# Performance work log

Hardware: AMD Instinct MI355X
Metric: run time of the kernel (lower is better)

Reference implementation:

```python
import jax, jax.numpy as jnp
import numpy as np

TOP_K_PERCENT = 0.25  # top_k_percent_pixels from init_kwargs
B, C, H, W = 8, 19, 512, 1024


def setup_inputs() -> dict:
    key = jax.random.key(0)
    k1, k2 = jax.random.split(key)
    logits = jax.random.normal(k1, (B, C, H, W), dtype=jnp.float32)
    labels = jax.random.randint(k2, (B, H, W), 0, C)  # int labels, in-range
    return {"logits": logits, "labels": labels}


def reference(logits, labels):
    # loss_fn: per-pixel cross-entropy with reduction='none' -> [B, H, W]
    logZ = jax.nn.logsumexp(logits, axis=1)  # [B, H, W], stable softmax normalizer
    gathered = jnp.take_along_axis(logits, labels[:, None, :, :], axis=1)[:, 0]  # [B, H, W]
    loss = logZ - gathered  # per-pixel CE
    # get_topk_percent: flatten non-batch dims, keep top k = pct * num_pixels per row
    flat = loss.reshape(loss.shape[0], -1)  # [B, H*W]
    num_pixels = flat.shape[1]
    k = int(TOP_K_PERCENT * num_pixels)
    top_vals, _ = jax.lax.top_k(flat, k)  # [B, k]
    return top_vals.mean()
```

## Files before the change

kernel.cpp:

```cpp
#include <hip/hip_runtime.h>
#include <cstdint>

#define BB   8
#define CC   19
#define HWP  524288
#define NPIX 4194304
#define KSEL 131072
#define GRID 4096

#define H1_OFF   0
#define H2_OFF   (8*2048)
#define H3_OFF   (H2_OFF + 8*4096)
#define SEL1_OFF (H3_OFF + 8*256)
#define CNT1_OFF (SEL1_OFF + 8)
#define SEL2_OFF (CNT1_OFF + 8)
#define CNT2_OFF (SEL2_OFF + 8)
#define PAD_OFF  (CNT2_OFF + 8)
#define SUMA_OFF (PAD_OFF + 4)
#define CTRL_WORDS (SUMA_OFF + 16)
#define LOSS_BYTES (NPIX * 4)


__device__ __forceinline__ uint32_t block_incl_scan_u32(uint32_t v, volatile uint32_t* wt) {
    int lane = threadIdx.x & 63, wid = threadIdx.x >> 6;
    uint32_t inc = v;
#pragma unroll
    for (int off = 1; off < 64; off <<= 1) {
        uint32_t t = __shfl_up(inc, off);
        if (lane >= off) inc += t;
    }
    __syncthreads();
    if (lane == 63) wt[wid] = inc;
    __syncthreads();
    for (int w = 0; w < wid; w++) inc += wt[w];
    return inc;
}

__device__ __forceinline__ double block_reduce_double(double v, volatile double* dwt) {
    int lane = threadIdx.x & 63, wid = threadIdx.x >> 6;
#pragma unroll
    for (int off = 32; off > 0; off >>= 1) v += __shfl_down(v, off);
    __syncthreads();
    if (lane == 0) dwt[wid] = v;
    __syncthreads();
    return dwt[0] + dwt[1] + dwt[2] + dwt[3];
}

__device__ __forceinline__ void block_sum_atomic(double sum, double* dst, volatile double* dwt) {
    double t = block_reduce_double(sum, dwt);
    if (threadIdx.x == 0 && t != 0.0) atomicAdd(dst, t);
}


__global__ __launch_bounds__(256) void loss_hist1(
    const float* __restrict__ logits, const int* __restrict__ labels,
    float* __restrict__ loss, uint32_t* __restrict__ hist1)
{
    __shared__ uint32_t lh[2048];
    for (int i = threadIdx.x; i < 2048; i += 256) lh[i] = 0u;
    __syncthreads();

    int b = blockIdx.x >> 9;
    int pix0 = blockIdx.x * 1024 + threadIdx.x * 4;
    int prow = pix0 & (HWP - 1);

    const float4* lg = (const float4*)(logits + (size_t)b * CC * HWP + prow);
    float4 a[CC];
#pragma unroll
    for (int c = 0; c < CC; c++) a[c] = lg[(size_t)c * (HWP / 4)];

    int4 lab = *(const int4*)(labels + pix0);

    float mx0 = a[0].x, mx1 = a[0].y, mx2 = a[0].z, mx3 = a[0].w;
#pragma unroll
    for (int c = 1; c < CC; c++) {
        mx0 = fmaxf(mx0, a[c].x); mx1 = fmaxf(mx1, a[c].y);
        mx2 = fmaxf(mx2, a[c].z); mx3 = fmaxf(mx3, a[c].w);
    }
    float g0 = 0.f, g1 = 0.f, g2 = 0.f, g3 = 0.f;
    float e0 = 0.f, e1 = 0.f, e2 = 0.f, e3 = 0.f;
#pragma unroll
    for (int c = 0; c < CC; c++) {
        e0 += __expf(a[c].x - mx0); e1 += __expf(a[c].y - mx1);
        e2 += __expf(a[c].z - mx2); e3 += __expf(a[c].w - mx3);
        g0 = (lab.x == c) ? a[c].x : g0;
        g1 = (lab.y == c) ? a[c].y : g1;
        g2 = (lab.z == c) ? a[c].z : g2;
        g3 = (lab.w == c) ? a[c].w : g3;
    }
    float l0 = fmaxf(mx0 + __logf(e0) - g0, 0.f);
    float l1 = fmaxf(mx1 + __logf(e1) - g1, 0.f);
    float l2 = fmaxf(mx2 + __logf(e2) - g2, 0.f);
    float l3 = fmaxf(mx3 + __logf(e3) - g3, 0.f);

    float4 o; o.x = l0; o.y = l1; o.z = l2; o.w = l3;
    *(float4*)(loss + pix0) = o;

    atomicAdd(&lh[__float_as_uint(l0) >> 20], 1u);
    atomicAdd(&lh[__float_as_uint(l1) >> 20], 1u);
    atomicAdd(&lh[__float_as_uint(l2) >> 20], 1u);
    atomicAdd(&lh[__float_as_uint(l3) >> 20], 1u);

    __syncthreads();
    for (int i = threadIdx.x; i < 2048; i += 256) {
        uint32_t v = lh[i];
        if (v) atomicAdd(&hist1[b * 2048 + i], v);
    }
}


template <int NBINS>
__global__ __launch_bounds__(256) void scan_k(
    const uint32_t* __restrict__ hist, const uint32_t* __restrict__ cntPrev,
    uint32_t* __restrict__ selOut, uint32_t* __restrict__ cntOut)
{
    __shared__ uint32_t wt[4];
    constexpr int CH = NBINS / 256;
    int r = blockIdx.x;
    const uint32_t* hrow = hist + r * NBINS;
    int base = NBINS - CH * ((int)threadIdx.x + 1);
    uint32_t hloc[CH];
    uint32_t csum = 0;
#pragma unroll
    for (int i = 0; i < CH; i++) { hloc[i] = hrow[base + i]; csum += hloc[i]; }
    uint32_t incl = block_incl_scan_u32(csum, wt);
    uint32_t pre = incl - csum;
    uint32_t prev = cntPrev ? cntPrev[r] : 0u;
    uint32_t target = (uint32_t)KSEL - prev;
    if (pre < target && pre + csum >= target) {
        uint32_t cum = pre;
#pragma unroll
        for (int i = CH - 1; i >= 0; i--) {
            uint32_t h = hloc[i];
            if (cum + h >= target) { selOut[r] = (uint32_t)(base + i); cntOut[r] = prev + cum; break; }
            cum += h;
        }
    }
}


__global__ __launch_bounds__(256) void refine2(
    const float* __restrict__ loss, uint32_t* __restrict__ hist2,
    const uint32_t* __restrict__ sel1, double* __restrict__ sumAbove)
{
    __shared__ uint32_t lh[4096];
    __shared__ double dwt[4];
    for (int i = threadIdx.x; i < 4096; i += 256) lh[i] = 0u;
    __syncthreads();

    int b = blockIdx.x >> 9;
    uint32_t s1 = sel1[b];
    int pix0 = blockIdx.x * 1024 + threadIdx.x * 4;
    float4 v = *(const float4*)(loss + pix0);

    double sum = 0.0;
    {
        float vv[4] = {v.x, v.y, v.z, v.w};
#pragma unroll
        for (int j = 0; j < 4; j++) {
            uint32_t u = __float_as_uint(vv[j]);
            uint32_t t = u >> 20;
            if (t > s1) sum += (double)vv[j];
            else if (t == s1) atomicAdd(&lh[(u >> 8) & 0xFFFu], 1u);
        }
    }
    __syncthreads();
    block_sum_atomic(sum, &sumAbove[b], dwt);
    for (int i = threadIdx.x; i < 4096; i += 256) {
        uint32_t c = lh[i];
        if (c) atomicAdd(&hist2[b * 4096 + i], c);
    }
}


__global__ __launch_bounds__(256) void refine3(
    const float* __restrict__ loss, uint32_t* __restrict__ hist3,
    const uint32_t* __restrict__ sel1, const uint32_t* __restrict__ sel2,
    double* __restrict__ sumAbove)
{
    __shared__ uint32_t lh[256];
    __shared__ double dwt[4];
    lh[threadIdx.x] = 0u;
    __syncthreads();

    int b = blockIdx.x >> 9;
    uint32_t s1 = sel1[b], s2 = sel2[b];
    int pix0 = blockIdx.x * 1024 + threadIdx.x * 4;
    float4 v = *(const float4*)(loss + pix0);

    double sum = 0.0;
    {
        float vv[4] = {v.x, v.y, v.z, v.w};
#pragma unroll
        for (int j = 0; j < 4; j++) {
            uint32_t u = __float_as_uint(vv[j]);
            if ((u >> 20) == s1) {
                uint32_t mid = (u >> 8) & 0xFFFu;
                if (mid > s2) sum += (double)vv[j];
                else if (mid == s2) atomicAdd(&lh[u & 0xFFu], 1u);
            }
        }
    }
    __syncthreads();
    block_sum_atomic(sum, &sumAbove[b], dwt);
    {
        uint32_t c = lh[threadIdx.x];
        if (c) atomicAdd(&hist3[b * 256 + threadIdx.x], c);
    }
}


__global__ __launch_bounds__(256) void finalize_k(
    const uint32_t* __restrict__ hist3,
    const uint32_t* __restrict__ sel1, const uint32_t* __restrict__ sel2,
    const uint32_t* __restrict__ cnt2, const double* __restrict__ sumAbove,
    float* __restrict__ out)
{
    __shared__ uint32_t wt[4];
    __shared__ double dwt[4];
    double tot = 0.0;
    for (int r = 0; r < BB; r++) {
        int b3 = 255 - (int)threadIdx.x;
        uint32_t h = hist3[r * 256 + b3];
        uint32_t incl = block_incl_scan_u32(h, wt);
        uint32_t pre = incl - h;
        uint32_t rem = (uint32_t)KSEL - cnt2[r];
        uint32_t take = (rem > pre) ? ((rem - pre < h) ? (rem - pre) : h) : 0u;
        uint32_t P = (sel1[r] << 20) | (sel2[r] << 8) | (uint32_t)b3;
        double contrib = (double)take * (double)__uint_as_float(P);
        double s = block_reduce_double(contrib, dwt);
        if (threadIdx.x == 0) tot += s + sumAbove[r];
    }
    if (threadIdx.x == 0) out[0] = (float)(tot / ((double)BB * (double)KSEL));
}

extern "C" void kernel_launch(void* const* d_in, const int* in_sizes, int n_in,
                              void* d_out, int out_size, void* d_ws, size_t ws_size,
                              hipStream_t stream)
{
    const float* logits = (const float*)d_in[0];
    const int* labels   = (const int*)d_in[1];
    float* out          = (float*)d_out;

    char* ws = (char*)d_ws;
    float* loss      = (float*)ws;
    uint32_t* ctrl   = (uint32_t*)(ws + LOSS_BYTES);
    uint32_t* hist1  = ctrl + H1_OFF;
    uint32_t* hist2  = ctrl + H2_OFF;
    uint32_t* hist3  = ctrl + H3_OFF;
    uint32_t* sel1   = ctrl + SEL1_OFF;
    uint32_t* cnt1   = ctrl + CNT1_OFF;
    uint32_t* sel2   = ctrl + SEL2_OFF;
    uint32_t* cnt2   = ctrl + CNT2_OFF;
    double* sumAbove = (double*)(ctrl + SUMA_OFF);

    (void)hipMemsetAsync(ctrl, 0, CTRL_WORDS * sizeof(uint32_t), stream);
    loss_hist1<<<GRID, 256, 0, stream>>>(logits, labels, loss, hist1);
    scan_k<2048><<<BB, 256, 0, stream>>>(hist1, nullptr, sel1, cnt1);
    refine2<<<GRID, 256, 0, stream>>>(loss, hist2, sel1, sumAbove);
    scan_k<4096><<<BB, 256, 0, stream>>>(hist2, cnt1, sel2, cnt2);
    refine3<<<GRID, 256, 0, stream>>>(loss, hist3, sel1, sel2, sumAbove);
    finalize_k<<<1, 256, 0, stream>>>(hist3, sel1, sel2, cnt2, sumAbove, out);
}
```

Measured before the change: 536.0 us.

## Fuse loss and radix-select passes into one cooperative persistent kernel

Replaces the six-launch pipeline with a single cooperative kernel of 512 blocks. Each block keeps its 8192 per-pixel losses in registers, and the stages are separated by grid.sync, so the loss buffer is never written to or re-read from global memory. Every block redoes the histogram scan for its own row instead of launching separate scan kernels, and the control words are zeroed inside the kernel rather than by a memset. The trade-offs are heavy register pressure from holding 19 float4 logits plus 8 float4 losses per thread, fewer blocks in flight to hide memory latency, and the cost of several grid-wide barriers; the old multi-kernel path stays as a fallback if the cooperative launch fails.

```diff
diff --git a/kernel.cpp b/kernel.cpp
--- a/kernel.cpp
+++ b/kernel.cpp
@@ -1,13 +1,23 @@
 #include <hip/hip_runtime.h>
+#include <hip/hip_cooperative_groups.h>
 #include <cstdint>
+
+namespace cg = cooperative_groups;
 
 #define BB   8
 #define CC   19
 #define HWP  524288
 #define NPIX 4194304
 #define KSEL 131072
+
+#define CNBLK 512
+#define CBPR  64
+#define CNTHR 256
+#define CGRP  8
+
 #define GRID 4096
 
+#define LOSS_BYTES (NPIX * 4)
 #define H1_OFF   0
 #define H2_OFF   (8*2048)
 #define H3_OFF   (H2_OFF + 8*4096)
@@ -16,9 +26,8 @@
 #define SEL2_OFF (CNT1_OFF + 8)
 #define CNT2_OFF (SEL2_OFF + 8)
 #define PAD_OFF  (CNT2_OFF + 8)
-#define SUMA_OFF (PAD_OFF + 4)
+#define SUMA_OFF (PAD_OFF + 2)
 #define CTRL_WORDS (SUMA_OFF + 16)
-#define LOSS_BYTES (NPIX * 4)
 
 
 __device__ __forceinline__ uint32_t block_incl_scan_u32(uint32_t v, volatile uint32_t* wt) {
@@ -49,6 +58,186 @@
 __device__ __forceinline__ void block_sum_atomic(double sum, double* dst, volatile double* dwt) {
     double t = block_reduce_double(sum, dwt);
     if (threadIdx.x == 0 && t != 0.0) atomicAdd(dst, t);
+}
+
+template <int NBINS>
+__device__ __forceinline__ void row_select(
+    const uint32_t* __restrict__ hrow, uint32_t prev,
+    volatile uint32_t* wt, volatile uint32_t* shSel, volatile uint32_t* shCnt,
+    uint32_t& sel, uint32_t& cnt)
+{
+    constexpr int CH = NBINS / 256;
+    int base = NBINS - CH * ((int)threadIdx.x + 1);
+    uint32_t hloc[CH];
+    uint32_t csum = 0;
+#pragma unroll
+    for (int i = 0; i < CH; i++) { hloc[i] = hrow[base + i]; csum += hloc[i]; }
+    uint32_t incl = block_incl_scan_u32(csum, wt);
+    uint32_t pre = incl - csum;
+    uint32_t target = (uint32_t)KSEL - prev;
+    if (pre < target && pre + csum >= target) {
+        uint32_t cum = pre;
+#pragma unroll
+        for (int i = CH - 1; i >= 0; i--) {
+            uint32_t h = hloc[i];
+            if (cum + h >= target) { *shSel = (uint32_t)(base + i); *shCnt = prev + cum; break; }
+            cum += h;
+        }
+    }
+    __syncthreads();
+    sel = *shSel; cnt = *shCnt;
+}
+
+
+__global__ __launch_bounds__(CNTHR, 2) void topk_ce_coop(
+    const float* __restrict__ logits, const int* __restrict__ labels,
+    uint32_t* __restrict__ ctrl, float* __restrict__ out)
+{
+    cg::grid_group grid = cg::this_grid();
+    __shared__ uint32_t lh[4096];
+    __shared__ uint32_t wt[4];
+    __shared__ double dwt[4];
+    __shared__ uint32_t shSel, shCnt;
+
+    uint32_t* hist1 = ctrl + H1_OFF;
+    uint32_t* hist2 = ctrl + H2_OFF;
+    uint32_t* hist3 = ctrl + H3_OFF;
+    uint32_t* sel1g = ctrl + SEL1_OFF;
+    uint32_t* sel2g = ctrl + SEL2_OFF;
+    uint32_t* cnt2g = ctrl + CNT2_OFF;
+    double* sumAbove = (double*)(ctrl + SUMA_OFF);
+
+    const int tid = threadIdx.x;
+    const int b = (int)blockIdx.x >> 6;
+    const int rowblk = (int)blockIdx.x & (CBPR - 1);
+
+    for (int i = (int)blockIdx.x * CNTHR + tid; i < CTRL_WORDS; i += CNBLK * CNTHR)
+        ctrl[i] = 0u;
+    for (int i = tid; i < 2048; i += CNTHR) lh[i] = 0u;
+    __syncthreads();
+
+    const size_t rowbase = (size_t)b * CC * HWP;
+    const size_t labbase = (size_t)b * HWP;
+    const int prow0 = rowblk * (CNTHR * 4 * CGRP) + tid * 4;
+
+    float4 lr[CGRP];
+#pragma unroll
+    for (int g = 0; g < CGRP; g++) {
+        const int prow = prow0 + g * (CNTHR * 4);
+        const float4* lg = (const float4*)(logits + rowbase + prow);
+        const int4 lab = *(const int4*)(labels + labbase + prow);
+        float4 a[CC];
+#pragma unroll
+        for (int c = 0; c < CC; c++) a[c] = lg[(size_t)c * (HWP / 4)];
+
+        float mx0 = a[0].x, mx1 = a[0].y, mx2 = a[0].z, mx3 = a[0].w;
+#pragma unroll
+        for (int c = 1; c < CC; c++) {
+            mx0 = fmaxf(mx0, a[c].x); mx1 = fmaxf(mx1, a[c].y);
+            mx2 = fmaxf(mx2, a[c].z); mx3 = fmaxf(mx3, a[c].w);
+        }
+        float g0 = 0.f, g1 = 0.f, g2 = 0.f, g3 = 0.f;
+        float e0 = 0.f, e1 = 0.f, e2 = 0.f, e3 = 0.f;
+#pragma unroll
+        for (int c = 0; c < CC; c++) {
+            e0 += __expf(a[c].x - mx0); e1 += __expf(a[c].y - mx1);
+            e2 += __expf(a[c].z - mx2); e3 += __expf(a[c].w - mx3);
+            g0 = (lab.x == c) ? a[c].x : g0;
+            g1 = (lab.y == c) ? a[c].y : g1;
+            g2 = (lab.z == c) ? a[c].z : g2;
+            g3 = (lab.w == c) ? a[c].w : g3;
+        }
+        float l0 = fmaxf(mx0 + __logf(e0) - g0, 0.f);
+        float l1 = fmaxf(mx1 + __logf(e1) - g1, 0.f);
+        float l2 = fmaxf(mx2 + __logf(e2) - g2, 0.f);
+        float l3 = fmaxf(mx3 + __logf(e3) - g3, 0.f);
+        lr[g] = make_float4(l0, l1, l2, l3);
+
+        atomicAdd(&lh[__float_as_uint(l0) >> 20], 1u);
+        atomicAdd(&lh[__float_as_uint(l1) >> 20], 1u);
+        atomicAdd(&lh[__float_as_uint(l2) >> 20], 1u);
+        atomicAdd(&lh[__float_as_uint(l3) >> 20], 1u);
+    }
+    __syncthreads();
+    grid.sync();
+    for (int i = tid; i < 2048; i += CNTHR) {
+        uint32_t v = lh[i];
+        if (v) atomicAdd(&hist1[b * 2048 + i], v);
+    }
+    grid.sync();
+
+    uint32_t sel1v, cnt1v;
+    row_select<2048>(hist1 + b * 2048, 0u, wt, &shSel, &shCnt, sel1v, cnt1v);
+    __syncthreads();
+    for (int i = tid; i < 4096; i += CNTHR) lh[i] = 0u;
+    __syncthreads();
+
+    double sum = 0.0;
+#pragma unroll
+    for (int g = 0; g < CGRP; g++) {
+        float vv[4] = {lr[g].x, lr[g].y, lr[g].z, lr[g].w};
+#pragma unroll
+        for (int j = 0; j < 4; j++) {
+            uint32_t u = __float_as_uint(vv[j]);
+            uint32_t t = u >> 20;
+            if (t > sel1v) sum += (double)vv[j];
+            else if (t == sel1v) atomicAdd(&lh[(u >> 8) & 0xFFFu], 1u);
+        }
+    }
+    __syncthreads();
+    block_sum_atomic(sum, &sumAbove[b], dwt);
+    for (int i = tid; i < 4096; i += CNTHR) {
+        uint32_t v = lh[i];
+        if (v) atomicAdd(&hist2[b * 4096 + i], v);
+    }
+    if (rowblk == 0 && tid == 0) sel1g[b] = sel1v;
+    grid.sync();
+
+    uint32_t sel2v, cnt2v;
+    row_select<4096>(hist2 + b * 4096, cnt1v, wt, &shSel, &shCnt, sel2v, cnt2v);
+    __syncthreads();
+    lh[tid] = 0u;
+    __syncthreads();
+
+    double sum2 = 0.0;
+#pragma unroll
+    for (int g = 0; g < CGRP; g++) {
+        float vv[4] = {lr[g].x, lr[g].y, lr[g].z, lr[g].w};
+#pragma unroll
+        for (int j = 0; j < 4; j++) {
+            uint32_t u = __float_as_uint(vv[j]);
+            if ((u >> 20) == sel1v) {
+                uint32_t mid = (u >> 8) & 0xFFFu;
+                if (mid > sel2v) sum2 += (double)vv[j];
+                else if (mid == sel2v) atomicAdd(&lh[u & 0xFFu], 1u);
+            }
+        }
+    }
+    __syncthreads();
+    block_sum_atomic(sum2, &sumAbove[b], dwt);
+    {
+        uint32_t c = lh[tid];
+        if (c) atomicAdd(&hist3[b * 256 + tid], c);
+    }
+    if (rowblk == 0 && tid == 0) { sel2g[b] = sel2v; cnt2g[b] = cnt2v; }
+    grid.sync();
+
+    if (blockIdx.x == 0) {
+        double tot = 0.0;
+        for (int r = 0; r < BB; r++) {
+            int b3 = 255 - tid;
+            uint32_t h = hist3[r * 256 + b3];
+            uint32_t incl = block_incl_scan_u32(h, wt);
+            uint32_t pre = incl - h;
+            uint32_t rem = (uint32_t)KSEL - cnt2g[r];
+            uint32_t take = (rem > pre) ? ((rem - pre < h) ? (rem - pre) : h) : 0u;
+            uint32_t P = (sel1g[r] << 20) | (sel2g[r] << 8) | (uint32_t)b3;
+            double contrib = (double)take * (double)__uint_as_float(P);
+            double s = block_reduce_double(contrib, dwt);
+            if (tid == 0) tot += s + sumAbove[r];
+        }
+        if (tid == 0) out[0] = (float)(tot / ((double)BB * (double)KSEL));
+    }
 }
 
 
@@ -108,7 +297,6 @@
     }
 }
 
-
 template <int NBINS>
 __global__ __launch_bounds__(256) void scan_k(
     const uint32_t* __restrict__ hist, const uint32_t* __restrict__ cntPrev,
@@ -138,7 +326,6 @@
     }
 }
 
-
 __global__ __launch_bounds__(256) void refine2(
     const float* __restrict__ loss, uint32_t* __restrict__ hist2,
     const uint32_t* __restrict__ sel1, double* __restrict__ sumAbove)
@@ -171,7 +358,6 @@
         if (c) atomicAdd(&hist2[b * 4096 + i], c);
     }
 }
-
 
 __global__ __launch_bounds__(256) void refine3(
     const float* __restrict__ loss, uint32_t* __restrict__ hist3,
@@ -208,7 +394,6 @@
         if (c) atomicAdd(&hist3[b * 256 + threadIdx.x], c);
     }
 }
-
 
 __global__ __launch_bounds__(256) void finalize_k(
     const uint32_t* __restrict__ hist3,
@@ -254,6 +439,18 @@
     uint32_t* cnt2   = ctrl + CNT2_OFF;
     double* sumAbove = (double*)(ctrl + SUMA_OFF);
 
+    {
+        const float* a0 = logits;
+        const int*   a1 = labels;
+        uint32_t*    a2 = ctrl;
+        float*       a3 = out;
+        void* args[4] = { (void*)&a0, (void*)&a1, (void*)&a2, (void*)&a3 };
+        if (hipLaunchCooperativeKernel(topk_ce_coop, dim3(CNBLK), dim3(CNTHR),
+                                       args, 0, stream) == hipSuccess)
+            return;
+        (void)hipGetLastError();
+    }
+
     (void)hipMemsetAsync(ctrl, 0, CTRL_WORDS * sizeof(uint32_t), stream);
     loss_hist1<<<GRID, 256, 0, stream>>>(logits, labels, loss, hist1);
     scan_k<2048><<<BB, 256, 0, stream>>>(hist1, nullptr, sel1, cnt1);
```

After: 669.4 us. 1.25x slower.

## Fold histogram scan-select into each refine kernel, dropping separate scan launches

Applied to the files above, without the earlier changes.

Removes the two small 8-block scan_k launches. Each block of the refine kernels now redundantly scans its row's histogram to find the selected bin, and block 0 of each row writes sel/cnt for later stages. This cuts two kernel launches and their serialization gaps, at the cost of every one of 4096 blocks re-reading and scanning a 2048- or 4096-entry histogram row. The SUMA offset shift keeps the double array 8-byte aligned.

```diff
diff --git a/kernel.cpp b/kernel.cpp
--- a/kernel.cpp
+++ b/kernel.cpp
@@ -16,7 +16,7 @@
 #define SEL2_OFF (CNT1_OFF + 8)
 #define CNT2_OFF (SEL2_OFF + 8)
 #define PAD_OFF  (CNT2_OFF + 8)
-#define SUMA_OFF (PAD_OFF + 4)
+#define SUMA_OFF (PAD_OFF + 2)
 #define CTRL_WORDS (SUMA_OFF + 16)
 #define LOSS_BYTES (NPIX * 4)
 
@@ -49,6 +49,34 @@
 __device__ __forceinline__ void block_sum_atomic(double sum, double* dst, volatile double* dwt) {
     double t = block_reduce_double(sum, dwt);
     if (threadIdx.x == 0 && t != 0.0) atomicAdd(dst, t);
+}
+
+template <int NBINS>
+__device__ __forceinline__ void row_select(
+    const uint32_t* __restrict__ hrow, uint32_t prev,
+    volatile uint32_t* wt, volatile uint32_t* shSel, volatile uint32_t* shCnt,
+    uint32_t& sel, uint32_t& cnt)
+{
+    constexpr int CH = NBINS / 256;
+    int base = NBINS - CH * ((int)threadIdx.x + 1);
+    uint32_t hloc[CH];
+    uint32_t csum = 0;
+#pragma unroll
+    for (int i = 0; i < CH; i++) { hloc[i] = hrow[base + i]; csum += hloc[i]; }
+    uint32_t incl = block_incl_scan_u32(csum, wt);
+    uint32_t pre = incl - csum;
+    uint32_t target = (uint32_t)KSEL - prev;
+    if (pre < target && pre + csum >= target) {
+        uint32_t cum = pre;
+#pragma unroll
+        for (int i = CH - 1; i >= 0; i--) {
+            uint32_t h = hloc[i];
+            if (cum + h >= target) { *shSel = (uint32_t)(base + i); *shCnt = prev + cum; break; }
+            cum += h;
+        }
+    }
+    __syncthreads();
+    sel = *shSel; cnt = *shCnt;
 }
 
 
@@ -109,47 +137,27 @@
 }
 
 
-template <int NBINS>
-__global__ __launch_bounds__(256) void scan_k(
-    const uint32_t* __restrict__ hist, const uint32_t* __restrict__ cntPrev,
-    uint32_t* __restrict__ selOut, uint32_t* __restrict__ cntOut)
-{
+__global__ __launch_bounds__(256) void refine2s(
+    const float* __restrict__ loss, const uint32_t* __restrict__ hist1,
+    uint32_t* __restrict__ hist2,
+    uint32_t* __restrict__ sel1g, uint32_t* __restrict__ cnt1g,
+    double* __restrict__ sumAbove)
+{
+    __shared__ uint32_t lh[4096];
     __shared__ uint32_t wt[4];
-    constexpr int CH = NBINS / 256;
-    int r = blockIdx.x;
-    const uint32_t* hrow = hist + r * NBINS;
-    int base = NBINS - CH * ((int)threadIdx.x + 1);
-    uint32_t hloc[CH];
-    uint32_t csum = 0;
-#pragma unroll
-    for (int i = 0; i < CH; i++) { hloc[i] = hrow[base + i]; csum += hloc[i]; }
-    uint32_t incl = block_incl_scan_u32(csum, wt);
-    uint32_t pre = incl - csum;
-    uint32_t prev = cntPrev ? cntPrev[r] : 0u;
-    uint32_t target = (uint32_t)KSEL - prev;
-    if (pre < target && pre + csum >= target) {
-        uint32_t cum = pre;
-#pragma unroll
-        for (int i = CH - 1; i >= 0; i--) {
-            uint32_t h = hloc[i];
-            if (cum + h >= target) { selOut[r] = (uint32_t)(base + i); cntOut[r] = prev + cum; break; }
-            cum += h;
-        }
-    }
-}
-
-
-__global__ __launch_bounds__(256) void refine2(
-    const float* __restrict__ loss, uint32_t* __restrict__ hist2,
-    const uint32_t* __restrict__ sel1, double* __restrict__ sumAbove)
-{
-    __shared__ uint32_t lh[4096];
     __shared__ double dwt[4];
+    __shared__ uint32_t shSel, shCnt;
     for (int i = threadIdx.x; i < 4096; i += 256) lh[i] = 0u;
     __syncthreads();
 
     int b = blockIdx.x >> 9;
-    uint32_t s1 = sel1[b];
+    int rowblk = blockIdx.x & 511;
+
+    uint32_t s1, c1;
+    row_select<2048>(hist1 + b * 2048, 0u, wt, &shSel, &shCnt, s1, c1);
+    if (rowblk == 0 && threadIdx.x == 0) { sel1g[b] = s1; cnt1g[b] = c1; }
+    __syncthreads();
+
     int pix0 = blockIdx.x * 1024 + threadIdx.x * 4;
     float4 v = *(const float4*)(loss + pix0);
 
@@ -173,18 +181,30 @@
 }
 
 
-__global__ __launch_bounds__(256) void refine3(
-    const float* __restrict__ loss, uint32_t* __restrict__ hist3,
-    const uint32_t* __restrict__ sel1, const uint32_t* __restrict__ sel2,
+__global__ __launch_bounds__(256) void refine3s(
+    const float* __restrict__ loss, const uint32_t* __restrict__ hist2,
+    uint32_t* __restrict__ hist3,
+    const uint32_t* __restrict__ sel1g, const uint32_t* __restrict__ cnt1g,
+    uint32_t* __restrict__ sel2g, uint32_t* __restrict__ cnt2g,
     double* __restrict__ sumAbove)
 {
     __shared__ uint32_t lh[256];
+    __shared__ uint32_t wt[4];
     __shared__ double dwt[4];
+    __shared__ uint32_t shSel, shCnt;
     lh[threadIdx.x] = 0u;
     __syncthreads();
 
     int b = blockIdx.x >> 9;
-    uint32_t s1 = sel1[b], s2 = sel2[b];
+    int rowblk = blockIdx.x & 511;
+    uint32_t s1 = sel1g[b];
+    uint32_t c1 = cnt1g[b];
+
+    uint32_t s2, c2;
+    row_select<4096>(hist2 + b * 4096, c1, wt, &shSel, &shCnt, s2, c2);
+    if (rowblk == 0 && threadIdx.x == 0) { sel2g[b] = s2; cnt2g[b] = c2; }
+    __syncthreads();
+
     int pix0 = blockIdx.x * 1024 + threadIdx.x * 4;
     float4 v = *(const float4*)(loss + pix0);
 
@@ -256,9 +276,7 @@
 
     (void)hipMemsetAsync(ctrl, 0, CTRL_WORDS * sizeof(uint32_t), stream);
     loss_hist1<<<GRID, 256, 0, stream>>>(logits, labels, loss, hist1);
-    scan_k<2048><<<BB, 256, 0, stream>>>(hist1, nullptr, sel1, cnt1);
-    refine2<<<GRID, 256, 0, stream>>>(loss, hist2, sel1, sumAbove);
-    scan_k<4096><<<BB, 256, 0, stream>>>(hist2, cnt1, sel2, cnt2);
-    refine3<<<GRID, 256, 0, stream>>>(loss, hist3, sel1, sel2, sumAbove);
+    refine2s<<<GRID, 256, 0, stream>>>(loss, hist1, hist2, sel1, cnt1, sumAbove);
+    refine3s<<<GRID, 256, 0, stream>>>(loss, hist2, hist3, sel1, cnt1, sel2, cnt2, sumAbove);
     finalize_k<<<1, 256, 0, stream>>>(hist3, sel1, sel2, cnt2, sumAbove, out);
 }
```

Result: no change. 541.6 us (+1.0%).
